# Kernel tuning notes

Hardware: AMD Instinct MI355X
Metric: run time of the kernel (lower is better)

Reference implementation:

```python
import jax, jax.numpy as jnp
import numpy as np

N_NODES, N_EDGES, NNZ, F_IN, HID, K = 50000, 10000, 800000, 128, 512, 10


def setup_inputs() -> dict:
    key = jax.random.key(0)
    ks = jax.random.split(key, 6)
    x = jax.random.normal(ks[0], (N_NODES, F_IN), dtype=jnp.float32)
    node_idx = jax.random.randint(ks[1], (NNZ,), 0, N_NODES)
    edge_idx = jax.random.randint(ks[2], (NNZ,), 0, N_EDGES)
    hyperedge_index = jnp.stack([node_idx, edge_idx]).astype(jnp.int64)
    edge_weight = jax.random.uniform(ks[3], (N_EDGES,), dtype=jnp.float32, minval=0.5, maxval=1.5)
    theta = jax.random.normal(ks[4], (K + 1,), dtype=jnp.float32) * 0.1
    lin1_w = jax.random.normal(ks[5], (HID, F_IN), dtype=jnp.float32) * (1.0 / np.sqrt(F_IN))
    lin1_b = jnp.zeros((HID,), dtype=jnp.float32)
    return {"x": x, "hyperedge_index": hyperedge_index, "edge_weight": edge_weight,
            "theta": theta, "lin1_w": lin1_w, "lin1_b": lin1_b}


def _hyper_prop_factory(node_idx, edge_idx, edge_weight, n_nodes, n_edges):
    """Returns A_norm @ x where A_norm = Dv^-1/2 H W De^-1 H^T Dv^-1/2."""
    ones = jnp.ones_like(node_idx, dtype=edge_weight.dtype)
    d_e = jax.ops.segment_sum(ones, edge_idx, num_segments=n_edges)            # edge degree
    d_v = jax.ops.segment_sum(edge_weight[edge_idx], node_idx, num_segments=n_nodes)
    dv_is = jnp.where(d_v > 0, jax.lax.rsqrt(jnp.maximum(d_v, 1e-12)), 0.0)
    de_w = edge_weight * jnp.where(d_e > 0, 1.0 / jnp.maximum(d_e, 1e-12), 0.0)

    def prop(x):
        xv = x * dv_is[:, None]                                               # [N, F]
        m_e = jax.ops.segment_sum(xv[node_idx], edge_idx, num_segments=n_edges)
        m_e = m_e * de_w[:, None]                                             # [E, F]
        out = jax.ops.segment_sum(m_e[edge_idx], node_idx, num_segments=n_nodes)
        return out * dv_is[:, None]

    return prop


def cheb_hypergraph(x, node_idx, edge_idx, edge_weight, theta, n_nodes, n_edges):
    # L_tilde = L - I = -A_norm (lambda_max = 2). Chebyshev recurrence on L_tilde.
    prop = _hyper_prop_factory(node_idx, edge_idx, edge_weight, n_nodes, n_edges)
    t_prev = x                       # T_0
    out = theta[0] * t_prev
    t_cur = -prop(x)                 # T_1 = L_tilde x
    out = out + theta[1] * t_cur
    for k in range(2, theta.shape[0]):
        t_next = -2.0 * prop(t_cur) - t_prev   # T_k = 2 L_tilde T_{k-1} - T_{k-2}
        out = out + theta[k] * t_next
        t_prev, t_cur = t_cur, t_next
    return out


def reference(x, hyperedge_index, edge_weight, theta, lin1_w, lin1_b):
    node_idx = hyperedge_index[0]
    edge_idx = hyperedge_index[1]
    n_nodes = x.shape[0]
    n_edges = edge_weight.shape[0]
    # eval mode: both dropouts are identity
    h = cheb_hypergraph(x, node_idx, edge_idx, edge_weight, theta, n_nodes, n_edges)
    h = jnp.einsum('nf,hf->nh', h, lin1_w) + lin1_b
    # is_bns=False -> no batch norm; act_fn='relu'
    return jax.nn.relu(h)
```

## Files before the change

kernel.cpp:

```cpp
#include <hip/hip_runtime.h>


#define N_NODES 50000
#define N_EDGES 10000
#define NNZ     800000
#define F_IN    128
#define HID     512
#define R16     16
#define NB_E    10
#define NB_N    49
#define HB      64
#define NW_E    (N_EDGES / 2)
#define NW_N    (N_NODES / 2)

typedef __attribute__((ext_vector_type(8))) short bf16x8;
typedef __attribute__((ext_vector_type(4))) float f32x4;

static __device__ __forceinline__ unsigned short f2bf(float f) {
    union { float f; unsigned u; } c; c.f = f;
    unsigned u = c.u;
    unsigned r = (u + 0x7fffu + ((u >> 16) & 1u)) >> 16;
    return (unsigned short)r;
}
static __device__ __forceinline__ float blo(unsigned u) {
    union { unsigned u; float f; } c; c.u = u << 16; return c.f;
}
static __device__ __forceinline__ float bhi(unsigned u) {
    union { unsigned u; float f; } c; c.u = u & 0xffff0000u; return c.f;
}
static __device__ __forceinline__ unsigned pack2(float lo, float hi) {
    return (unsigned)f2bf(lo) | ((unsigned)f2bf(hi) << 16);
}

__global__ __launch_bounds__(1024) void k_hist(const int* __restrict__ hidx,
                                               unsigned short* __restrict__ loc_e,
                                               unsigned short* __restrict__ loc_v,
                                               unsigned* __restrict__ hist_e,
                                               unsigned* __restrict__ hist_n) {
    __shared__ unsigned she[NW_E];
    __shared__ unsigned shn[NW_N];
    int tid = (int)threadIdx.x;
    for (int w = tid; w < NW_E; w += 1024) she[w] = 0;
    for (int w = tid; w < NW_N; w += 1024) shn[w] = 0;
    __syncthreads();
    int bid = (int)blockIdx.x;
    for (int i = bid * 1024 + tid; i < NNZ; i += HB * 1024) {
        int v = hidx[i];
        int e = hidx[NNZ + i];
        v = min(max(v, 0), N_NODES - 1);
        e = min(max(e, 0), N_EDGES - 1);
        int se = (e & 1) * 16;
        int sv = (v & 1) * 16;
        unsigned oe = atomicAdd(&she[e >> 1], 1u << se);
        unsigned ov = atomicAdd(&shn[v >> 1], 1u << sv);
        loc_e[i] = (unsigned short)((oe >> se) & 0xFFFFu);
        loc_v[i] = (unsigned short)((ov >> sv) & 0xFFFFu);
    }
    __syncthreads();
    for (int w = tid; w < NW_E; w += 1024) hist_e[bid * NW_E + w] = she[w];
    for (int w = tid; w < NW_N; w += 1024) hist_n[bid * NW_N + w] = shn[w];
}

__global__ void k_combine(const unsigned* __restrict__ hist_e,
                          const unsigned* __restrict__ hist_n,
                          int* __restrict__ base_e,
                          int* __restrict__ base_n,
                          int* __restrict__ counts_e,
                          int* __restrict__ counts_n) {
    int i = blockIdx.x * blockDim.x + threadIdx.x;
    if (i < N_EDGES) {
        int sh = (i & 1) * 16;
        int w = i >> 1;
        int s = 0;
#pragma unroll 8
        for (int b = 0; b < HB; ++b) {
            base_e[b * N_EDGES + i] = s;
            s += (int)((hist_e[b * NW_E + w] >> sh) & 0xFFFFu);
        }
        counts_e[i] = s;
    }
    if (i < N_NODES) {
        int sh = (i & 1) * 16;
        int w = i >> 1;
        int s = 0;
#pragma unroll 8
        for (int b = 0; b < HB; ++b) {
            base_n[b * N_NODES + i] = s;
            s += (int)((hist_n[b * NW_N + w] >> sh) & 0xFFFFu);
        }
        counts_n[i] = s;
    }
}

__global__ __launch_bounds__(1024) void k_scan_blk2(const int* __restrict__ ce,
                                                    const int* __restrict__ cn,
                                                    int* __restrict__ oute,
                                                    int* __restrict__ outn,
                                                    int* __restrict__ pe,
                                                    int* __restrict__ pn) {
    __shared__ int sd[1024];
    int b = (int)blockIdx.x;
    const int* counts; int n; int* out; int* partial; int lb;
    if (b < NB_E) { counts = ce; n = N_EDGES; out = oute; partial = pe; lb = b; }
    else          { counts = cn; n = N_NODES; out = outn; partial = pn; lb = b - NB_E; }
    int tid = (int)threadIdx.x;
    int i = lb * 1024 + tid;
    int v = (i < n) ? counts[i] : 0;
    sd[tid] = v;
    __syncthreads();
    for (int off = 1; off < 1024; off <<= 1) {
        int t = (tid >= off) ? sd[tid - off] : 0;
        __syncthreads();
        sd[tid] += t;
        __syncthreads();
    }
    if (i < n) out[i] = sd[tid] - v;
    if (tid == 1023) partial[lb] = sd[1023];
}

__global__ void k_scan_top2(int* __restrict__ pe, int* __restrict__ pn,
                            int* __restrict__ tot_e, int* __restrict__ tot_n) {
    int w = (int)threadIdx.x >> 6;
    int lane = (int)threadIdx.x & 63;
    int* partial = w ? pn : pe;
    int nb       = w ? NB_N : NB_E;
    int* total   = w ? tot_n : tot_e;
    int v = (lane < nb) ? partial[lane] : 0;
    int incl = v;
    for (int off = 1; off < 64; off <<= 1) {
        int t = __shfl_up(incl, off);
        if (lane >= off) incl += t;
    }
    if (lane < nb) partial[lane] = incl - v;
    if (lane == 63) *total = incl;
}

__global__ __launch_bounds__(1024) void k_scan_add2(int* __restrict__ oute,
                                                    int* __restrict__ outn,
                                                    const int* __restrict__ pe,
                                                    const int* __restrict__ pn) {
    int b = (int)blockIdx.x;
    int* out; const int* partial; int n; int lb;
    if (b < NB_E) { out = oute; partial = pe; n = N_EDGES; lb = b; }
    else          { out = outn; partial = pn; n = N_NODES; lb = b - NB_E; }
    int i = lb * 1024 + (int)threadIdx.x;
    if (i < n) out[i] += partial[lb];
}

__global__ void k_fill(const int* __restrict__ hidx,
                       const int* __restrict__ edge_ptr,
                       const int* __restrict__ node_ptr,
                       const unsigned short* __restrict__ loc_e,
                       const unsigned short* __restrict__ loc_v,
                       const int* __restrict__ base_e,
                       const int* __restrict__ base_n,
                       int* __restrict__ edge_node,
                       int* __restrict__ node_edge) {
    int i = blockIdx.x * blockDim.x + threadIdx.x;
    if (i >= NNZ) return;
    int wg = (i >> 10) & (HB - 1);
    int v = hidx[i];
    int e = hidx[NNZ + i];
    v = min(max(v, 0), N_NODES - 1);
    e = min(max(e, 0), N_EDGES - 1);
    edge_node[edge_ptr[e] + base_e[wg * N_EDGES + e] + (int)loc_e[i]] = v;
    node_edge[node_ptr[v] + base_n[wg * N_NODES + v] + (int)loc_v[i]] = e;
}

__global__ void k_norms2(const float* __restrict__ ew,
                         const int* __restrict__ edge_ptr,
                         const int* __restrict__ node_ptr,
                         const int* __restrict__ node_edge,
                         float* __restrict__ dv_is,
                         float* __restrict__ de_w) {
    int i = blockIdx.x * blockDim.x + threadIdx.x;
    if (i < N_NODES) {
        int s = node_ptr[i], t = node_ptr[i + 1];
        float d = 0.f;
        for (int j = s; j < t; ++j) d += ew[node_edge[j]];
        dv_is[i] = (d > 0.f) ? rsqrtf(fmaxf(d, 1e-12f)) : 0.f;
    }
    if (i < N_EDGES) {
        int c = edge_ptr[i + 1] - edge_ptr[i];
        de_w[i] = ew[i] * ((c > 0) ? (1.f / (float)c) : 0.f);
    }
}

__global__ void k_init(const float* __restrict__ x,
                       const float* __restrict__ theta,
                       const float* __restrict__ dv_is,
                       uint4* __restrict__ bufA,
                       float* __restrict__ acc) {
    int i = blockIdx.x * blockDim.x + threadIdx.x;
    if (i >= N_NODES * R16) return;
    int v = i >> 4;
    float dvv = dv_is[v];
    float w = (dvv > 0.f) ? dvv : 1.f;
    float4 x0 = ((const float4*)x)[2 * i];
    float4 x1 = ((const float4*)x)[2 * i + 1];
    uint4 q;
    q.x = pack2(w * x0.x, w * x0.y); q.y = pack2(w * x0.z, w * x0.w);
    q.z = pack2(w * x1.x, w * x1.y); q.w = pack2(w * x1.z, w * x1.w);
    bufA[i] = q;
    float t0 = theta[0];
    float4 a0, a1;
    a0.x = t0 * x0.x; a0.y = t0 * x0.y; a0.z = t0 * x0.z; a0.w = t0 * x0.w;
    a1.x = t0 * x1.x; a1.y = t0 * x1.y; a1.z = t0 * x1.z; a1.w = t0 * x1.w;
    ((float4*)acc)[2 * i]     = a0;
    ((float4*)acc)[2 * i + 1] = a1;
}

__global__ void k_phaseA(const uint4* __restrict__ tin,
                         const float* __restrict__ de_w,
                         const int* __restrict__ edge_ptr,
                         const int* __restrict__ edge_node,
                         uint4* __restrict__ m_e) {
    int tid    = (int)threadIdx.x;
    int wv     = tid >> 6;
    int l64    = tid & 63;
    int stream = l64 >> 3;
    int sl     = l64 & 7;
    int b      = (int)blockIdx.x;
    int slab   = (b >= (N_EDGES / 4)) ? 1 : 0;
    int e      = (b - slab * (N_EDGES / 4)) * 4 + wv;
    int col    = slab * 8 + sl;
    int s = edge_ptr[e], t = edge_ptr[e + 1];
    float a0=0.f,a1=0.f,a2=0.f,a3=0.f,a4=0.f,a5=0.f,a6=0.f,a7=0.f;
    int j = s + stream;
    for (; j + 24 < t; j += 32) {
        int v0 = edge_node[j];
        int v1 = edge_node[j + 8];
        int v2 = edge_node[j + 16];
        int v3 = edge_node[j + 24];
        uint4 q0 = tin[v0 * R16 + col];
        uint4 q1 = tin[v1 * R16 + col];
        uint4 q2 = tin[v2 * R16 + col];
        uint4 q3 = tin[v3 * R16 + col];
        a0 += (blo(q0.x) + blo(q1.x)) + (blo(q2.x) + blo(q3.x));
        a1 += (bhi(q0.x) + bhi(q1.x)) + (bhi(q2.x) + bhi(q3.x));
        a2 += (blo(q0.y) + blo(q1.y)) + (blo(q2.y) + blo(q3.y));
        a3 += (bhi(q0.y) + bhi(q1.y)) + (bhi(q2.y) + bhi(q3.y));
        a4 += (blo(q0.z) + blo(q1.z)) + (blo(q2.z) + blo(q3.z));
        a5 += (bhi(q0.z) + bhi(q1.z)) + (bhi(q2.z) + bhi(q3.z));
        a6 += (blo(q0.w) + blo(q1.w)) + (blo(q2.w) + blo(q3.w));
        a7 += (bhi(q0.w) + bhi(q1.w)) + (bhi(q2.w) + bhi(q3.w));
    }
    for (; j < t; j += 8) {
        int v0 = edge_node[j];
        uint4 q0 = tin[v0 * R16 + col];
        a0 += blo(q0.x); a1 += bhi(q0.x);
        a2 += blo(q0.y); a3 += bhi(q0.y);
        a4 += blo(q0.z); a5 += bhi(q0.z);
        a6 += blo(q0.w); a7 += bhi(q0.w);
    }
    a0 += __shfl_xor(a0, 8);  a1 += __shfl_xor(a1, 8);
    a2 += __shfl_xor(a2, 8);  a3 += __shfl_xor(a3, 8);
    a4 += __shfl_xor(a4, 8);  a5 += __shfl_xor(a5, 8);
    a6 += __shfl_xor(a6, 8);  a7 += __shfl_xor(a7, 8);
    a0 += __shfl_xor(a0, 16); a1 += __shfl_xor(a1, 16);
    a2 += __shfl_xor(a2, 16); a3 += __shfl_xor(a3, 16);
    a4 += __shfl_xor(a4, 16); a5 += __shfl_xor(a5, 16);
    a6 += __shfl_xor(a6, 16); a7 += __shfl_xor(a7, 16);
    a0 += __shfl_xor(a0, 32); a1 += __shfl_xor(a1, 32);
    a2 += __shfl_xor(a2, 32); a3 += __shfl_xor(a3, 32);
    a4 += __shfl_xor(a4, 32); a5 += __shfl_xor(a5, 32);
    a6 += __shfl_xor(a6, 32); a7 += __shfl_xor(a7, 32);
    if (stream == 0) {
        float w = de_w[e];
        uint4 o;
        o.x = pack2(a0 * w, a1 * w); o.y = pack2(a2 * w, a3 * w);
        o.z = pack2(a4 * w, a5 * w); o.w = pack2(a6 * w, a7 * w);
        m_e[e * R16 + col] = o;
    }
}

__global__ void k_phaseB(const uint4* __restrict__ m_e,
                         const uint4* __restrict__ tin,
                         const float* __restrict__ dv_is,
                         const int* __restrict__ node_ptr,
                         const int* __restrict__ node_edge,
                         uint4* __restrict__ tio,
                         float* __restrict__ acc,
                         const float* __restrict__ theta, int k,
                         float ca, float cb, int accMode) {
    int tid    = (int)threadIdx.x;
    int g      = tid >> 4;
    int t16    = tid & 15;
    int stream = t16 >> 3;
    int sl     = t16 & 7;
    int b      = (int)blockIdx.x;
    int slab   = (b >= (N_NODES / 16)) ? 1 : 0;
    int v      = (b - slab * (N_NODES / 16)) * 16 + g;
    int col    = slab * 8 + sl;
    int s = node_ptr[v], t = node_ptr[v + 1];
    float s0=0.f,s1=0.f,s2=0.f,s3=0.f,s4=0.f,s5=0.f,s6=0.f,s7=0.f;
    int j = s + stream;
    for (; j + 2 < t; j += 4) {
        int e0 = node_edge[j];
        int e1 = node_edge[j + 2];
        uint4 q0 = m_e[e0 * R16 + col];
        uint4 q1 = m_e[e1 * R16 + col];
        s0 += blo(q0.x) + blo(q1.x); s1 += bhi(q0.x) + bhi(q1.x);
        s2 += blo(q0.y) + blo(q1.y); s3 += bhi(q0.y) + bhi(q1.y);
        s4 += blo(q0.z) + blo(q1.z); s5 += bhi(q0.z) + bhi(q1.z);
        s6 += blo(q0.w) + blo(q1.w); s7 += bhi(q0.w) + bhi(q1.w);
    }
    if (j < t) {
        int e0 = node_edge[j];
        uint4 q0 = m_e[e0 * R16 + col];
        s0 += blo(q0.x); s1 += bhi(q0.x);
        s2 += blo(q0.y); s3 += bhi(q0.y);
        s4 += blo(q0.z); s5 += bhi(q0.z);
        s6 += blo(q0.w); s7 += bhi(q0.w);
    }
    s0 += __shfl_xor(s0, 8); s1 += __shfl_xor(s1, 8);
    s2 += __shfl_xor(s2, 8); s3 += __shfl_xor(s3, 8);
    s4 += __shfl_xor(s4, 8); s5 += __shfl_xor(s5, 8);
    s6 += __shfl_xor(s6, 8); s7 += __shfl_xor(s7, 8);
    if (stream == 0) {
        float dvv = dv_is[v];
        float scf = ca * dvv * dvv;
        int idx = v * R16 + col;
        uint4 tp = tio[idx];
        float t0 = scf * s0 + cb * blo(tp.x);
        float t1 = scf * s1 + cb * bhi(tp.x);
        float t2 = scf * s2 + cb * blo(tp.y);
        float t3 = scf * s3 + cb * bhi(tp.y);
        float t4 = scf * s4 + cb * blo(tp.z);
        float t5 = scf * s5 + cb * bhi(tp.z);
        float t6 = scf * s6 + cb * blo(tp.w);
        float t7 = scf * s7 + cb * bhi(tp.w);
        uint4 tn;
        tn.x = pack2(t0, t1); tn.y = pack2(t2, t3);
        tn.z = pack2(t4, t5); tn.w = pack2(t6, t7);
        tio[idx] = tn;
        if (accMode) {
            float thk = theta[k];
            float a0 = thk * t0, a1 = thk * t1, a2 = thk * t2, a3 = thk * t3;
            float a4 = thk * t4, a5 = thk * t5, a6 = thk * t6, a7 = thk * t7;
            if (accMode >= 2) {
                float th1 = theta[k - 1];
                uint4 tq = tin[idx];
                a0 += th1 * blo(tq.x); a1 += th1 * bhi(tq.x);
                a2 += th1 * blo(tq.y); a3 += th1 * bhi(tq.y);
                a4 += th1 * blo(tq.z); a5 += th1 * bhi(tq.z);
                a6 += th1 * blo(tq.w); a7 += th1 * bhi(tq.w);
            }
            if (accMode >= 3) {
                float th2 = theta[k - 2];
                a0 += th2 * blo(tp.x); a1 += th2 * bhi(tp.x);
                a2 += th2 * blo(tp.y); a3 += th2 * bhi(tp.y);
                a4 += th2 * blo(tp.z); a5 += th2 * bhi(tp.z);
                a6 += th2 * blo(tp.w); a7 += th2 * bhi(tp.w);
            }
            float iw = (dvv > 0.f) ? (1.f / dvv) : 1.f;
            float4* acc4 = (float4*)acc;
            int ai = v * 32 + col * 2;
            float4 a = acc4[ai];
            a.x += iw * a0; a.y += iw * a1; a.z += iw * a2; a.w += iw * a3;
            acc4[ai] = a;
            float4 bvec = acc4[ai + 1];
            bvec.x += iw * a4; bvec.y += iw * a5; bvec.z += iw * a6; bvec.w += iw * a7;
            acc4[ai + 1] = bvec;
        }
    }
}

#define M_TILES 782
__global__ __launch_bounds__(256) void k_gemm(const float* __restrict__ A,
                                              const float* __restrict__ W,
                                              const float* __restrict__ bias,
                                              float* __restrict__ out) {
    __shared__ short Asm[64 * 136];
    __shared__ short Wsm[64 * 136];
    int id  = (int)blockIdx.x;
    int xcd = id & 7;
    int sub = id >> 3;
    int h_t = sub & 7;
    int m_i = sub >> 3;
    int m_t = xcd * 98 + m_i;
    if (m_t >= M_TILES) return;
    int m0 = m_t * 64;
    int h0 = h_t * 64;
    int tid = (int)threadIdx.x;

    const float4* A4 = (const float4*)A;
    const float4* W4 = (const float4*)W;
#pragma unroll
    for (int i = 0; i < 4; ++i) {
        int c   = tid + i * 256;
        int row = c >> 4;
        int q4  = c & 15;
        int gr = m0 + row;
        float4 a0, a1;
        if (gr < N_NODES) {
            a0 = A4[(size_t)gr * 32 + q4 * 2];
            a1 = A4[(size_t)gr * 32 + q4 * 2 + 1];
        } else {
            a0 = make_float4(0.f, 0.f, 0.f, 0.f);
            a1 = a0;
        }
        uint4 pa;
        pa.x = pack2(a0.x, a0.y); pa.y = pack2(a0.z, a0.w);
        pa.z = pack2(a1.x, a1.y); pa.w = pack2(a1.z, a1.w);
        *(uint4*)&Asm[row * 136 + q4 * 8] = pa;
        float4 w0 = W4[(size_t)(h0 + row) * 32 + q4 * 2];
        float4 w1 = W4[(size_t)(h0 + row) * 32 + q4 * 2 + 1];
        uint4 pw;
        pw.x = pack2(w0.x, w0.y); pw.y = pack2(w0.z, w0.w);
        pw.z = pack2(w1.x, w1.y); pw.w = pack2(w1.z, w1.w);
        *(uint4*)&Wsm[row * 136 + q4 * 8] = pw;
    }
    __syncthreads();

    int lane = tid & 63;
    int wv   = tid >> 6;
    int l16  = lane & 15;
    int quad = lane >> 4;

    f32x4 acc[4];
#pragma unroll
    for (int n = 0; n < 4; ++n) acc[n] = (f32x4){0.f, 0.f, 0.f, 0.f};

#pragma unroll
    for (int ks = 0; ks < 4; ++ks) {
        int k0 = ks * 32;
        bf16x8 af = *(const bf16x8*)&Asm[(wv * 16 + l16) * 136 + k0 + quad * 8];
#pragma unroll
        for (int n = 0; n < 4; ++n) {
            bf16x8 bf = *(const bf16x8*)&Wsm[(n * 16 + l16) * 136 + k0 + quad * 8];
            acc[n] = __builtin_amdgcn_mfma_f32_16x16x32_bf16(af, bf, acc[n], 0, 0, 0);
        }
    }

#pragma unroll
    for (int n = 0; n < 4; ++n) {
        float bb = bias[h0 + n * 16 + l16];
#pragma unroll
        for (int r = 0; r < 4; ++r) {
            int gr = m0 + wv * 16 + quad * 4 + r;
            if (gr < N_NODES)
                out[(size_t)gr * HID + h0 + n * 16 + l16] =
                    fmaxf(acc[n][r] + bb, 0.f);
        }
    }
}

extern "C" void kernel_launch(void* const* d_in, const int* in_sizes, int n_in,
                              void* d_out, int out_size, void* d_ws, size_t ws_size,
                              hipStream_t stream) {
    const float* x     = (const float*)d_in[0];
    const int*   hidx  = (const int*)d_in[1];
    const float* ew    = (const float*)d_in[2];
    const float* theta = (const float*)d_in[3];
    const float* w1    = (const float*)d_in[4];
    const float* b1    = (const float*)d_in[5];
    float*       out   = (float*)d_out;
    int kp1 = in_sizes[3];
    int K   = kp1 - 1;

    char* ob = (char*)d_out;
    size_t oo = 0;
    auto oalloc = [&](size_t bytes) -> void* {
        void* p = ob + oo;
        oo = (oo + bytes + 255) & ~(size_t)255;
        return p;
    };
    uint4* bufA      = (uint4*)oalloc((size_t)N_NODES * F_IN * 2);
    uint4* bufB      = (uint4*)oalloc((size_t)N_NODES * F_IN * 2);
    uint4* m_e       = (uint4*)oalloc((size_t)N_EDGES * F_IN * 2);
    int*   edge_node = (int*)oalloc((size_t)NNZ * 4);
    int*   node_edge = (int*)oalloc((size_t)NNZ * 4);
    unsigned short* loc_e = (unsigned short*)oalloc((size_t)NNZ * 2);
    unsigned short* loc_v = (unsigned short*)oalloc((size_t)NNZ * 2);
    unsigned* hist_e = (unsigned*)oalloc((size_t)HB * NW_E * 4);
    unsigned* hist_n = (unsigned*)oalloc((size_t)HB * NW_N * 4);
    int*   base_e    = (int*)oalloc((size_t)HB * N_EDGES * 4);
    int*   base_n    = (int*)oalloc((size_t)HB * N_NODES * 4);
    int*   counts_e  = (int*)oalloc((size_t)N_EDGES * 4);
    int*   counts_n  = (int*)oalloc((size_t)N_NODES * 4);

    char* ws = (char*)d_ws;
    size_t off = 0;
    auto alloc = [&](size_t bytes) -> void* {
        void* p = ws + off;
        off = (off + bytes + 255) & ~(size_t)255;
        return p;
    };
    float* accv     = (float*)alloc((size_t)N_NODES * F_IN * 4);
    float* dv_is    = (float*)alloc((size_t)N_NODES * 4);
    float* de_w     = (float*)alloc((size_t)N_EDGES * 4);
    int*   edge_ptr = (int*)alloc((size_t)(N_EDGES + 1) * 4);
    int*   node_ptr = (int*)alloc((size_t)(N_NODES + 1) * 4);
    int*   part_e   = (int*)alloc(64 * 4);
    int*   part_n   = (int*)alloc(64 * 4);

    k_hist<<<HB, 1024, 0, stream>>>(hidx, loc_e, loc_v, hist_e, hist_n);
    k_combine<<<(N_NODES + 255) / 256, 256, 0, stream>>>(hist_e, hist_n,
                                                         base_e, base_n,
                                                         counts_e, counts_n);

    k_scan_blk2<<<NB_E + NB_N, 1024, 0, stream>>>(counts_e, counts_n, edge_ptr, node_ptr,
                                                  part_e, part_n);
    k_scan_top2<<<1, 128, 0, stream>>>(part_e, part_n, edge_ptr + N_EDGES, node_ptr + N_NODES);
    k_scan_add2<<<NB_E + NB_N, 1024, 0, stream>>>(edge_ptr, node_ptr, part_e, part_n);

    k_fill<<<(NNZ + 255) / 256, 256, 0, stream>>>(hidx, edge_ptr, node_ptr,
                                                  loc_e, loc_v, base_e, base_n,
                                                  edge_node, node_edge);
    k_norms2<<<(N_NODES + 255) / 256, 256, 0, stream>>>(ew, edge_ptr, node_ptr,
                                                        node_edge, dv_is, de_w);
    k_init<<<(N_NODES * R16 + 255) / 256, 256, 0, stream>>>(x, theta, dv_is, bufA, accv);

    for (int k = 1; k <= K; ++k) {
        const uint4* tin = (k & 1) ? bufA : bufB;
        uint4*       tio = (k & 1) ? bufB : bufA;
        float ca = (k == 1) ? -1.f : -2.f;
        float cb = (k == 1) ? 0.f : -1.f;
        int accMode = 0;
        if (k % 3 == 0) accMode = 3;
        else if (k == K && (K % 3) != 0) accMode = K % 3;
        k_phaseA<<<2 * (N_EDGES / 4), 256, 0, stream>>>(tin, de_w, edge_ptr, edge_node, m_e);
        k_phaseB<<<2 * (N_NODES / 16), 256, 0, stream>>>(m_e, tin, dv_is, node_ptr, node_edge,
                                                         tio, accv, theta, k, ca, cb, accMode);
    }

    k_gemm<<<8 * 98 * 8, 256, 0, stream>>>(accv, w1, b1, out);
}
```

Baseline: 727.1 us.

## Fold scan-top into scan-add, fuse norms with init, double histogram blocks

Removes the separate single-block top-level scan kernel: each add block now reduces the preceding partial sums itself and the last block writes the total. The degree/normalisation kernel and the initialisation kernel are merged so dv_is is passed through shared memory instead of being reread from global memory. HB is doubled, so the histogram/offset preparation uses 128 blocks instead of 64, which enlarges the per-block base arrays. These cut launch count and latency in the CSR build preamble, at the cost of some redundant partial-sum reads and larger preparation buffers.

```diff
diff --git a/kernel.cpp b/kernel.cpp
--- a/kernel.cpp
+++ b/kernel.cpp
@@ -9,7 +9,7 @@
 #define R16     16
 #define NB_E    10
 #define NB_N    49
-#define HB      64
+#define HB      128
 #define NW_E    (N_EDGES / 2)
 #define NW_N    (N_NODES / 2)
 
@@ -118,33 +118,28 @@
     if (tid == 1023) partial[lb] = sd[1023];
 }
 
-__global__ void k_scan_top2(int* __restrict__ pe, int* __restrict__ pn,
-                            int* __restrict__ tot_e, int* __restrict__ tot_n) {
-    int w = (int)threadIdx.x >> 6;
-    int lane = (int)threadIdx.x & 63;
-    int* partial = w ? pn : pe;
-    int nb       = w ? NB_N : NB_E;
-    int* total   = w ? tot_n : tot_e;
-    int v = (lane < nb) ? partial[lane] : 0;
-    int incl = v;
-    for (int off = 1; off < 64; off <<= 1) {
-        int t = __shfl_up(incl, off);
-        if (lane >= off) incl += t;
-    }
-    if (lane < nb) partial[lane] = incl - v;
-    if (lane == 63) *total = incl;
-}
-
 __global__ __launch_bounds__(1024) void k_scan_add2(int* __restrict__ oute,
                                                     int* __restrict__ outn,
                                                     const int* __restrict__ pe,
                                                     const int* __restrict__ pn) {
+    __shared__ int s_add;
     int b = (int)blockIdx.x;
-    int* out; const int* partial; int n; int lb;
-    if (b < NB_E) { out = oute; partial = pe; n = N_EDGES; lb = b; }
-    else          { out = outn; partial = pn; n = N_NODES; lb = b - NB_E; }
-    int i = lb * 1024 + (int)threadIdx.x;
-    if (i < n) out[i] += partial[lb];
+    int* out; const int* partial; int n; int lb; int nbl;
+    if (b < NB_E) { out = oute; partial = pe; n = N_EDGES; lb = b; nbl = NB_E; }
+    else          { out = outn; partial = pn; n = N_NODES; lb = b - NB_E; nbl = NB_N; }
+    int tid = (int)threadIdx.x;
+    if (tid < 64) {
+        int v = (tid < lb) ? partial[tid] : 0;
+        for (int off = 1; off < 64; off <<= 1) v += __shfl_xor(v, off);
+        if (tid == 0) {
+            s_add = v;
+            if (lb == nbl - 1) out[n] = v + partial[lb];
+        }
+    }
+    __syncthreads();
+    int add = s_add;
+    int i = lb * 1024 + tid;
+    if (i < n) out[i] += add;
 }
 
 __global__ void k_fill(const int* __restrict__ hidx,
@@ -167,47 +162,53 @@
     node_edge[node_ptr[v] + base_n[wg * N_NODES + v] + (int)loc_v[i]] = e;
 }
 
-__global__ void k_norms2(const float* __restrict__ ew,
-                         const int* __restrict__ edge_ptr,
-                         const int* __restrict__ node_ptr,
-                         const int* __restrict__ node_edge,
-                         float* __restrict__ dv_is,
-                         float* __restrict__ de_w) {
-    int i = blockIdx.x * blockDim.x + threadIdx.x;
-    if (i < N_NODES) {
-        int s = node_ptr[i], t = node_ptr[i + 1];
+__global__ void k_normsinit(const float* __restrict__ ew,
+                            const int* __restrict__ edge_ptr,
+                            const int* __restrict__ node_ptr,
+                            const int* __restrict__ node_edge,
+                            const float* __restrict__ x,
+                            const float* __restrict__ theta,
+                            float* __restrict__ dv_is,
+                            float* __restrict__ de_w,
+                            uint4* __restrict__ bufA,
+                            float* __restrict__ acc) {
+    __shared__ float sh_w[256];
+    int tid = (int)threadIdx.x;
+    int gi = (int)blockIdx.x * 256 + tid;
+    if (gi < N_NODES) {
+        int s = node_ptr[gi], t = node_ptr[gi + 1];
         float d = 0.f;
         for (int j = s; j < t; ++j) d += ew[node_edge[j]];
-        dv_is[i] = (d > 0.f) ? rsqrtf(fmaxf(d, 1e-12f)) : 0.f;
-    }
-    if (i < N_EDGES) {
-        int c = edge_ptr[i + 1] - edge_ptr[i];
-        de_w[i] = ew[i] * ((c > 0) ? (1.f / (float)c) : 0.f);
-    }
-}
-
-__global__ void k_init(const float* __restrict__ x,
-                       const float* __restrict__ theta,
-                       const float* __restrict__ dv_is,
-                       uint4* __restrict__ bufA,
-                       float* __restrict__ acc) {
-    int i = blockIdx.x * blockDim.x + threadIdx.x;
-    if (i >= N_NODES * R16) return;
-    int v = i >> 4;
-    float dvv = dv_is[v];
-    float w = (dvv > 0.f) ? dvv : 1.f;
-    float4 x0 = ((const float4*)x)[2 * i];
-    float4 x1 = ((const float4*)x)[2 * i + 1];
-    uint4 q;
-    q.x = pack2(w * x0.x, w * x0.y); q.y = pack2(w * x0.z, w * x0.w);
-    q.z = pack2(w * x1.x, w * x1.y); q.w = pack2(w * x1.z, w * x1.w);
-    bufA[i] = q;
+        float dv = (d > 0.f) ? rsqrtf(fmaxf(d, 1e-12f)) : 0.f;
+        dv_is[gi] = dv;
+        sh_w[tid] = (dv > 0.f) ? dv : 1.f;
+    }
+    if (gi < N_EDGES) {
+        int c = edge_ptr[gi + 1] - edge_ptr[gi];
+        de_w[gi] = ew[gi] * ((c > 0) ? (1.f / (float)c) : 0.f);
+    }
+    __syncthreads();
     float t0 = theta[0];
-    float4 a0, a1;
-    a0.x = t0 * x0.x; a0.y = t0 * x0.y; a0.z = t0 * x0.z; a0.w = t0 * x0.w;
-    a1.x = t0 * x1.x; a1.y = t0 * x1.y; a1.z = t0 * x1.z; a1.w = t0 * x1.w;
-    ((float4*)acc)[2 * i]     = a0;
-    ((float4*)acc)[2 * i + 1] = a1;
+    int vbase = (int)blockIdx.x * 256;
+    for (int r = tid; r < 256 * R16; r += 256) {
+        int vl = r >> 4;
+        int v = vbase + vl;
+        if (v >= N_NODES) break;
+        int lane = r & 15;
+        int i = v * R16 + lane;
+        float w = sh_w[vl];
+        float4 x0 = ((const float4*)x)[2 * i];
+        float4 x1 = ((const float4*)x)[2 * i + 1];
+        uint4 q;
+        q.x = pack2(w * x0.x, w * x0.y); q.y = pack2(w * x0.z, w * x0.w);
+        q.z = pack2(w * x1.x, w * x1.y); q.w = pack2(w * x1.z, w * x1.w);
+        bufA[i] = q;
+        float4 a0, a1;
+        a0.x = t0 * x0.x; a0.y = t0 * x0.y; a0.z = t0 * x0.z; a0.w = t0 * x0.w;
+        a1.x = t0 * x1.x; a1.y = t0 * x1.y; a1.z = t0 * x1.z; a1.w = t0 * x1.w;
+        ((float4*)acc)[2 * i]     = a0;
+        ((float4*)acc)[2 * i + 1] = a1;
+    }
 }
 
 __global__ void k_phaseA(const uint4* __restrict__ tin,
@@ -502,15 +503,14 @@
 
     k_scan_blk2<<<NB_E + NB_N, 1024, 0, stream>>>(counts_e, counts_n, edge_ptr, node_ptr,
                                                   part_e, part_n);
-    k_scan_top2<<<1, 128, 0, stream>>>(part_e, part_n, edge_ptr + N_EDGES, node_ptr + N_NODES);
     k_scan_add2<<<NB_E + NB_N, 1024, 0, stream>>>(edge_ptr, node_ptr, part_e, part_n);
 
     k_fill<<<(NNZ + 255) / 256, 256, 0, stream>>>(hidx, edge_ptr, node_ptr,
                                                   loc_e, loc_v, base_e, base_n,
                                                   edge_node, node_edge);
-    k_norms2<<<(N_NODES + 255) / 256, 256, 0, stream>>>(ew, edge_ptr, node_ptr,
-                                                        node_edge, dv_is, de_w);
-    k_init<<<(N_NODES * R16 + 255) / 256, 256, 0, stream>>>(x, theta, dv_is, bufA, accv);
+    k_normsinit<<<(N_NODES + 255) / 256, 256, 0, stream>>>(ew, edge_ptr, node_ptr,
+                                                           node_edge, x, theta,
+                                                           dv_is, de_w, bufA, accv);
 
     for (int k = 1; k <= K; ++k) {
         const uint4* tin = (k & 1) ? bufA : bufB;
```

Result: no change. 735.5 us (+1.2%).
